# Optimization experiments

Hardware: AMD Instinct MI355X
Metric: run time of the kernel (lower is better)

Reference implementation:

```python
import jax, jax.numpy as jnp
import numpy as np

H, W = 512, 1024            # panorama resolution
GRID = 512                  # occupancy histogram resolution (height=width=512)
ABS_SCALE = 20000.0         # mm, ground-plane extent
UNIT_SCALE = 1000.0         # m -> mm
COUNT_TH = 100.0            # histogram count clamp


def _xyz_sphere(ref_plan):
    # Vectorized version of the original double loop.
    i = np.arange(H, dtype=np.float32)
    j = np.arange(W, dtype=np.float32)
    theta = -np.pi * (i / (H - 1) - 0.5)          # [H]
    phi = np.pi * (2.0 * j / (W - 1) - 1.0)       # [W]
    ct, st = np.cos(theta)[:, None], np.sin(theta)[:, None]   # [H,1]
    cp, sp = np.cos(phi)[None, :], np.sin(phi)[None, :]       # [1,W]
    if ref_plan == 'horizontal':
        P = np.stack([cp * ct, sp * ct, np.broadcast_to(st, (H, W))], 0)
    elif ref_plan == 'vertical':
        P = np.stack([cp * ct, np.broadcast_to(-st, (H, W)), sp * ct], 0)
    else:  # lateral
        P = np.stack([sp * ct, np.broadcast_to(-st, (H, W)), cp * ct], 0)
    return jnp.asarray(P.astype(np.float32))      # [3,H,W]

_SPHERES = [_xyz_sphere(p) for p in ('horizontal', 'vertical', 'lateral')]


def _density_one(depth_hw, sph):
    # depth_hw: [H,W]; sph: [3,H,W]
    ps = depth_hw[None] * sph                               # [3,H,W] 3D points
    xy = ps[:2].reshape(2, -1) * UNIT_SCALE                 # [2,N] mm, (x,y)
    coords = (xy + ABS_SCALE / 2.0) / ABS_SCALE * GRID      # [2,N] in grid units
    coords = jnp.clip(jnp.round(coords), 0.0, GRID - 1).astype(jnp.int32)
    flat = coords[1] * GRID + coords[0]                     # density[y, x]
    hist = jnp.zeros(GRID * GRID, jnp.float32).at[flat].add(1.0)
    hist = jnp.minimum(hist, COUNT_TH)
    hist = hist / jnp.max(hist)
    return hist.reshape(GRID, GRID)


def _density(depth, sph):
    # depth: [B,1,H,W] -> [B,GRID,GRID], batched scatter histogram
    return jax.vmap(_density_one, in_axes=(0, None))(depth[:, 0], sph)


def _inverse_huber(pred, gt):
    # berHu loss: L1 below c = 0.2*max|d|, scaled L2 above.
    diff = jnp.abs(pred - gt)
    c = 0.2 * jnp.max(diff)
    loss = jnp.where(diff <= c, diff, (diff * diff + c * c) / (2.0 * c))
    return jnp.mean(loss)


def setup_inputs() -> dict:
    key = jax.random.key(0)
    k1, k2 = jax.random.split(key)
    # indoor depths in [0, 10) meters so histogram bins are populated
    pred = jax.random.uniform(k1, (16, 1, H, W), jnp.float32) * 10.0
    gt = jax.random.uniform(k2, (16, 1, H, W), jnp.float32) * 10.0
    return {"pred_depth": pred, "gt_depth": gt}


def reference(pred_depth, gt_depth):
    total = jnp.float32(0.0)
    for sph in _SPHERES:  # fixed 3 projection planes
        pred_om = _density(pred_depth, sph)
        gt_om = _density(gt_depth, sph)
        total = total + _inverse_huber(pred_om, gt_om)
    return total
```

## Files before the change

kernel.cpp:

```cpp
#include <hip/hip_runtime.h>

#define PI_F 3.14159265358979323846f

#define MAXZ_OFF_B   24576
#define HIST_OFF_B   32768
#define BINS_OFF_B   25198592

__device__ inline float div20000(float a) {
    const float r = 1.0f / 20000.0f;
    float q0 = a * r;
    float e = fmaf(-20000.0f, q0, a);
    return fmaf(e, r, q0);
}

__device__ inline int bin1(float v) {
    float f = rintf(div20000(v + 10000.0f) * 512.0f);
    return (int)fminf(fmaxf(f, 0.0f), 511.0f);
}

__global__ __launch_bounds__(256) void bin_kernel(
    const float* __restrict__ pred, const float* __restrict__ gt,
    unsigned* __restrict__ bins, unsigned* __restrict__ maxz,
    float* __restrict__ out) {
    __shared__ float sct[4], sst[4];
    const int tid = threadIdx.x, wg = blockIdx.x;
    const int xcd = wg & 7, i4 = (wg >> 3) & 127, hh = wg >> 10;
    const int h = (hh << 3) | xcd;
    if (wg == 0) {
        if (tid < 128) maxz[tid] = 0u;
        if (tid == 128) out[0] = 0.0f;
    }
    if (tid < 4) {
        float fi = (float)(i4 * 4 + tid);
        float theta = -PI_F * (fi / 511.0f - 0.5f);
        sct[tid] = cosf(theta);
        sst[tid] = sinf(theta);
    }
    float cp[4], sp[4];
    #pragma unroll
    for (int k = 0; k < 4; ++k) {
        float fj = (float)(tid * 4 + k);
        float phi = PI_F * ((2.0f * fj) / 1023.0f - 1.0f);
        cp[k] = cosf(phi);
        sp[k] = sinf(phi);
    }
    __syncthreads();
    const float* img = ((h >> 4) ? gt : pred) + ((h & 15) << 19);
    #pragma unroll
    for (int r = 0; r < 4; ++r) {
        const int i = i4 * 4 + r;
        const float4 d4 = *(const float4*)(img + (i << 10) + (tid << 2));
        const float ct = sct[r], st = sst[r];
        uint4 o;
        #pragma unroll
        for (int k = 0; k < 4; ++k) {
            float d = (&d4.x)[k];
            float aA = cp[k] * ct;
            float aB = sp[k] * ct;
            float A = (d * aA) * 1000.0f;
            float B = (d * aB) * 1000.0f;
            float C = (d * (-st)) * 1000.0f;
            int iA = bin1(A), iB = bin1(B), iC = bin1(C);
            (&o.x)[k] = ((unsigned)iC << 18) | ((unsigned)iB << 9) | (unsigned)iA;
        }
        *(uint4*)(bins + ((unsigned)h << 19) + (i << 10) + (tid << 2)) = o;
    }
}

__global__ __launch_bounds__(1024, 8) void scan_kernel(
    const unsigned* __restrict__ bins, unsigned* __restrict__ hp,
    unsigned* __restrict__ maxraw) {
    __shared__ unsigned lh[16384];
    __shared__ unsigned s4[16];
    const int tid = threadIdx.x, wg = blockIdx.x;
    const int xcd = wg & 7, hhi = (wg >> 3) & 3;
    const int X = wg >> 5;
    const int pair = X / 6, idx6 = X % 6;
    const int plane = idx6 >> 1;
    const int band = (idx6 & 1) ? (4 + pair) : (3 - pair);
    const int h = (hhi << 3) | xcd;

    #pragma unroll
    for (int k = 0; k < 4; ++k)
        *(uint4*)&lh[(k << 12) + (tid << 2)] = make_uint4(0, 0, 0, 0);
    __syncthreads();

    int rlo, rhi;
    if (plane == 0) {
        float g = fmaxf(193.0f - 64.0f * band, 64.0f * band - 256.0f);
        float cmin = (g - 4.0f) * (1.0f / 256.0f);
        if (cmin <= 0.0f) { rlo = 0; rhi = 512; }
        else {
            float L = 511.0f * acosf(fminf(cmin, 1.0f)) / PI_F;
            rlo = max(0, (int)floorf(255.5f - L) - 3);
            rhi = min(512, (int)ceilf(255.5f + L) + 4);
        }
    } else if (band == 3) { rlo = 0; rhi = 260; }
    else if (band == 4) { rlo = 0; rhi = 512; }
    else if (band < 3) {
        float smin = (189.0f - 64.0f * band) * (1.0f / 256.0f);
        rlo = 0;
        rhi = min(512, (int)ceilf(511.0f * (0.5f - asinf(smin) / PI_F)) + 4);
    } else {
        float smin = (64.0f * band - 260.0f) * (1.0f / 256.0f);
        rhi = 512;
        rlo = max(0, (int)floorf(511.0f * (0.5f + asinf(smin) / PI_F)) - 4);
    }

    int s1, m1, m2, bsh;
    if (plane == 0)      { s1 = 0; m1 = 0x7FFF; m2 = 0;   bsh = 15; }
    else if (plane == 1) { s1 = 9; m1 = 0x7E00; m2 = 511; bsh = 24; }
    else                 { s1 = 9; m1 = 0x7FFF; m2 = 0;   bsh = 24; }
    const unsigned bandu = (unsigned)band;
    const unsigned* src = bins + ((unsigned)h << 19);

    auto process = [&](uint4 v) {
        #pragma unroll
        for (int k = 0; k < 4; ++k) {
            unsigned b = (&v.x)[k];
            if (((b >> bsh) & 7u) == bandu) {
                unsigned id = ((b >> s1) & m1) | (b & m2);
                atomicAdd(&lh[id >> 1], 1u << ((id & 1u) << 4));
            }
        }
    };

    const int t4 = (tid & 255) << 2;
    const int rof = tid >> 8;
    int r = rlo + rof;
    uint4 cur = make_uint4(0u, 0u, 0u, 0u);
    if (r < rhi) cur = *(const uint4*)&src[(r << 10) + t4];
    for (int rbase = rlo; rbase < rhi; rbase += 4) {
        int rn = rbase + 4 + rof;
        uint4 nxt = make_uint4(0u, 0u, 0u, 0u);
        if (rn < rhi) nxt = *(const uint4*)&src[(rn << 10) + t4];
        if (rbase + rof < rhi) process(cur);
        cur = nxt;
    }
    __syncthreads();

    unsigned m = 0;
    unsigned* gout = hp + ((plane * 32 + h) << 16) + (band << 13);
    #pragma unroll
    for (int k = 0; k < 8; ++k) {
        int w = (k << 10) + tid;
        unsigned v0 = lh[2 * w], v1 = lh[2 * w + 1];
        unsigned c0 = v0 & 65535u, c1 = v0 >> 16;
        unsigned c2 = v1 & 65535u, c3 = v1 >> 16;
        m = max(max(m, max(c0, c1)), max(c2, c3));
        gout[w] = min(c0, 255u) | (min(c1, 255u) << 8) |
                  (min(c2, 255u) << 16) | (min(c3, 255u) << 24);
    }
    #pragma unroll
    for (int o = 32; o; o >>= 1) m = max(m, (unsigned)__shfl_down((int)m, o));
    if ((tid & 63) == 0) s4[tid >> 6] = m;
    __syncthreads();
    if (tid == 0) {
        #pragma unroll
        for (int k = 1; k < 16; ++k) m = max(m, s4[k]);
        atomicMax(&maxraw[plane * 32 + h], m);
    }
}

__device__ inline float blockMaxF(float v) {
    #pragma unroll
    for (int o = 32; o; o >>= 1) v = fmaxf(v, __shfl_down(v, o));
    __shared__ float s[4];
    if ((threadIdx.x & 63) == 0) s[threadIdx.x >> 6] = v;
    __syncthreads();
    if (threadIdx.x == 0) v = fmaxf(fmaxf(s[0], s[1]), fmaxf(s[2], s[3]));
    return v;
}

__device__ inline float blockSumF(float v) {
    #pragma unroll
    for (int o = 32; o; o >>= 1) v += __shfl_down(v, o);
    __shared__ float s[4];
    if ((threadIdx.x & 63) == 0) s[threadIdx.x >> 6] = v;
    __syncthreads();
    if (threadIdx.x == 0) v = (s[0] + s[1]) + (s[2] + s[3]);
    return v;
}

__global__ void maxdiff_kernel(const unsigned* __restrict__ hp,
                               const unsigned* __restrict__ maxraw,
                               unsigned* __restrict__ maxdiff) {
    int blk = blockIdx.x;
    int b = blk & 15, chunk = (blk >> 4) & 15, plane = blk >> 8;
    const unsigned* P = hp + ((plane * 32 + b) << 16) + (chunk << 12);
    const unsigned* G = P + (16 << 16);
    float nP = fminf((float)maxraw[plane * 32 + b], 100.0f);
    float nG = fminf((float)maxraw[plane * 32 + 16 + b], 100.0f);
    float m = 0.0f;
    #pragma unroll
    for (int k = 0; k < 4; ++k) {
        uint4 wp = *(const uint4*)&P[(k << 10) + (threadIdx.x << 2)];
        uint4 wg = *(const uint4*)&G[(k << 10) + (threadIdx.x << 2)];
        #pragma unroll
        for (int w = 0; w < 4; ++w) {
            unsigned up = (&wp.x)[w], ug = (&wg.x)[w];
            #pragma unroll
            for (int s = 0; s < 32; s += 8) {
                float pn = fminf((float)((up >> s) & 255u), 100.0f) / nP;
                float gn = fminf((float)((ug >> s) & 255u), 100.0f) / nG;
                m = fmaxf(m, fabsf(pn - gn));
            }
        }
    }
    m = blockMaxF(m);
    if (threadIdx.x == 0) atomicMax(&maxdiff[plane], __float_as_uint(m));
}

__global__ void loss_kernel(const unsigned* __restrict__ hp,
                            const unsigned* __restrict__ maxraw,
                            const unsigned* __restrict__ maxdiff,
                            float* __restrict__ out) {
    int blk = blockIdx.x;
    int b = blk & 15, chunk = (blk >> 4) & 15, plane = blk >> 8;
    const unsigned* P = hp + ((plane * 32 + b) << 16) + (chunk << 12);
    const unsigned* G = P + (16 << 16);
    float c = 0.2f * __uint_as_float(maxdiff[plane]);
    float nP = fminf((float)maxraw[plane * 32 + b], 100.0f);
    float nG = fminf((float)maxraw[plane * 32 + 16 + b], 100.0f);
    float acc = 0.0f;
    #pragma unroll
    for (int k = 0; k < 4; ++k) {
        uint4 wp = *(const uint4*)&P[(k << 10) + (threadIdx.x << 2)];
        uint4 wg = *(const uint4*)&G[(k << 10) + (threadIdx.x << 2)];
        #pragma unroll
        for (int w = 0; w < 4; ++w) {
            unsigned up = (&wp.x)[w], ug = (&wg.x)[w];
            #pragma unroll
            for (int s = 0; s < 32; s += 8) {
                float pn = fminf((float)((up >> s) & 255u), 100.0f) / nP;
                float gn = fminf((float)((ug >> s) & 255u), 100.0f) / nG;
                float d = fabsf(pn - gn);
                acc += (d <= c) ? d : (d * d + c * c) / (2.0f * c);
            }
        }
    }
    acc = blockSumF(acc);
    if (threadIdx.x == 0) atomicAdd(out, acc / 4194304.0f);
}

extern "C" void kernel_launch(void* const* d_in, const int* in_sizes, int n_in,
                              void* d_out, int out_size, void* d_ws, size_t ws_size,
                              hipStream_t stream) {
    const float* pred = (const float*)d_in[0];
    const float* gt   = (const float*)d_in[1];
    float* out        = (float*)d_out;
    char* ws          = (char*)d_ws;

    unsigned* maxz    = (unsigned*)(ws + MAXZ_OFF_B);
    unsigned* maxraw  = maxz;
    unsigned* maxdiff = maxz + 96;
    unsigned* hp      = (unsigned*)(ws + HIST_OFF_B);
    unsigned* bins    = (unsigned*)(ws + BINS_OFF_B);

    bin_kernel<<<4096, 256, 0, stream>>>(pred, gt, bins, maxz, out);
    scan_kernel<<<768, 1024, 0, stream>>>(bins, hp, maxraw);
    maxdiff_kernel<<<768, 256, 0, stream>>>(hp, maxraw, maxdiff);
    loss_kernel<<<768, 256, 0, stream>>>(hp, maxraw, maxdiff, out);
}
```

Before: 219.8 us.

## Bucket binned indices per plane/band in bin kernel instead of packed bins

The bin kernel now counting-sorts each pixel's three plane indices into 24 plane/band buckets per workgroup, using shared-memory atomic counters, and writes compact 16-bit ids into a per-workgroup region with an offset header. The scan kernel then reads only its own bucket's ids from each of 128 regions instead of streaming whole image rows and filtering by band. This removes the redundant full-row reads and the acos/asin-based row-range logic. In exchange it adds shared atomics and a 48-entry register array in the bin kernel, plus scattered 16-bit global writes.

```diff
diff --git a/kernel.cpp b/kernel.cpp
--- a/kernel.cpp
+++ b/kernel.cpp
@@ -4,7 +4,8 @@
 
 #define MAXZ_OFF_B   24576
 #define HIST_OFF_B   32768
-#define BINS_OFF_B   25198592
+#define BUCK_OFF_B   25198592
+#define REGION_U16   12320
 
 __device__ inline float div20000(float a) {
     const float r = 1.0f / 20000.0f;
@@ -20,9 +21,11 @@
 
 __global__ __launch_bounds__(256) void bin_kernel(
     const float* __restrict__ pred, const float* __restrict__ gt,
-    unsigned* __restrict__ bins, unsigned* __restrict__ maxz,
+    unsigned short* __restrict__ buck, unsigned* __restrict__ maxz,
     float* __restrict__ out) {
     __shared__ float sct[4], sst[4];
+    __shared__ unsigned cnt[24];
+    __shared__ unsigned off[25];
     const int tid = threadIdx.x, wg = blockIdx.x;
     const int xcd = wg & 7, i4 = (wg >> 3) & 127, hh = wg >> 10;
     const int h = (hh << 3) | xcd;
@@ -30,6 +33,7 @@
         if (tid < 128) maxz[tid] = 0u;
         if (tid == 128) out[0] = 0.0f;
     }
+    if (tid < 24) cnt[tid] = 0u;
     if (tid < 4) {
         float fi = (float)(i4 * 4 + tid);
         float theta = -PI_F * (fi / 511.0f - 0.5f);
@@ -46,12 +50,12 @@
     }
     __syncthreads();
     const float* img = ((h >> 4) ? gt : pred) + ((h & 15) << 19);
+    unsigned items[48];
     #pragma unroll
     for (int r = 0; r < 4; ++r) {
         const int i = i4 * 4 + r;
         const float4 d4 = *(const float4*)(img + (i << 10) + (tid << 2));
         const float ct = sct[r], st = sst[r];
-        uint4 o;
         #pragma unroll
         for (int k = 0; k < 4; ++k) {
             float d = (&d4.x)[k];
@@ -61,14 +65,42 @@
             float B = (d * aB) * 1000.0f;
             float C = (d * (-st)) * 1000.0f;
             int iA = bin1(A), iB = bin1(B), iC = bin1(C);
-            (&o.x)[k] = ((unsigned)iC << 18) | ((unsigned)iB << 9) | (unsigned)iA;
-        }
-        *(uint4*)(bins + ((unsigned)h << 19) + (i << 10) + (tid << 2)) = o;
+            unsigned b0 = (unsigned)(iB >> 6);
+            unsigned b1 = 8u + (unsigned)(iC >> 6);
+            unsigned b2 = 16u + (unsigned)(iC >> 6);
+            unsigned id0 = ((unsigned)(iB & 63) << 9) | (unsigned)iA;
+            unsigned id1 = ((unsigned)(iC & 63) << 9) | (unsigned)iA;
+            unsigned id2 = ((unsigned)(iC & 63) << 9) | (unsigned)iB;
+            unsigned r0 = atomicAdd(&cnt[b0], 1u);
+            unsigned r1 = atomicAdd(&cnt[b1], 1u);
+            unsigned r2 = atomicAdd(&cnt[b2], 1u);
+            const int base = (r * 4 + k) * 3;
+            items[base + 0] = (b0 << 27) | (r0 << 15) | id0;
+            items[base + 1] = (b1 << 27) | (r1 << 15) | id1;
+            items[base + 2] = (b2 << 27) | (r2 << 15) | id2;
+        }
+    }
+    __syncthreads();
+    if (tid == 0) {
+        unsigned s = 0;
+        #pragma unroll
+        for (int b = 0; b < 24; ++b) { off[b] = s; s += cnt[b]; }
+        off[24] = s;
+    }
+    __syncthreads();
+    unsigned short* reg = buck + (size_t)wg * REGION_U16;
+    if (tid < 25) reg[tid] = (unsigned short)off[tid];
+    unsigned short* data = reg + 32;
+    #pragma unroll
+    for (int t = 0; t < 48; ++t) {
+        const unsigned it = items[t];
+        data[off[it >> 27] + ((it >> 15) & 4095u)] =
+            (unsigned short)(it & 32767u);
     }
 }
 
 __global__ __launch_bounds__(1024, 8) void scan_kernel(
-    const unsigned* __restrict__ bins, unsigned* __restrict__ hp,
+    const unsigned short* __restrict__ buck, unsigned* __restrict__ hp,
     unsigned* __restrict__ maxraw) {
     __shared__ unsigned lh[16384];
     __shared__ unsigned s4[16];
@@ -79,63 +111,23 @@
     const int plane = idx6 >> 1;
     const int band = (idx6 & 1) ? (4 + pair) : (3 - pair);
     const int h = (hhi << 3) | xcd;
+    const int bucket = plane * 8 + band;
 
     #pragma unroll
     for (int k = 0; k < 4; ++k)
         *(uint4*)&lh[(k << 12) + (tid << 2)] = make_uint4(0, 0, 0, 0);
     __syncthreads();
 
-    int rlo, rhi;
-    if (plane == 0) {
-        float g = fmaxf(193.0f - 64.0f * band, 64.0f * band - 256.0f);
-        float cmin = (g - 4.0f) * (1.0f / 256.0f);
-        if (cmin <= 0.0f) { rlo = 0; rhi = 512; }
-        else {
-            float L = 511.0f * acosf(fminf(cmin, 1.0f)) / PI_F;
-            rlo = max(0, (int)floorf(255.5f - L) - 3);
-            rhi = min(512, (int)ceilf(255.5f + L) + 4);
-        }
-    } else if (band == 3) { rlo = 0; rhi = 260; }
-    else if (band == 4) { rlo = 0; rhi = 512; }
-    else if (band < 3) {
-        float smin = (189.0f - 64.0f * band) * (1.0f / 256.0f);
-        rlo = 0;
-        rhi = min(512, (int)ceilf(511.0f * (0.5f - asinf(smin) / PI_F)) + 4);
-    } else {
-        float smin = (64.0f * band - 260.0f) * (1.0f / 256.0f);
-        rhi = 512;
-        rlo = max(0, (int)floorf(511.0f * (0.5f + asinf(smin) / PI_F)) - 4);
-    }
-
-    int s1, m1, m2, bsh;
-    if (plane == 0)      { s1 = 0; m1 = 0x7FFF; m2 = 0;   bsh = 15; }
-    else if (plane == 1) { s1 = 9; m1 = 0x7E00; m2 = 511; bsh = 24; }
-    else                 { s1 = 9; m1 = 0x7FFF; m2 = 0;   bsh = 24; }
-    const unsigned bandu = (unsigned)band;
-    const unsigned* src = bins + ((unsigned)h << 19);
-
-    auto process = [&](uint4 v) {
-        #pragma unroll
-        for (int k = 0; k < 4; ++k) {
-            unsigned b = (&v.x)[k];
-            if (((b >> bsh) & 7u) == bandu) {
-                unsigned id = ((b >> s1) & m1) | (b & m2);
-                atomicAdd(&lh[id >> 1], 1u << ((id & 1u) << 4));
-            }
-        }
-    };
-
-    const int t4 = (tid & 255) << 2;
-    const int rof = tid >> 8;
-    int r = rlo + rof;
-    uint4 cur = make_uint4(0u, 0u, 0u, 0u);
-    if (r < rhi) cur = *(const uint4*)&src[(r << 10) + t4];
-    for (int rbase = rlo; rbase < rhi; rbase += 4) {
-        int rn = rbase + 4 + rof;
-        uint4 nxt = make_uint4(0u, 0u, 0u, 0u);
-        if (rn < rhi) nxt = *(const uint4*)&src[(rn << 10) + t4];
-        if (rbase + rof < rhi) process(cur);
-        cur = nxt;
+    const int wid = tid >> 6, lane = tid & 63;
+    for (int i4 = wid; i4 < 128; i4 += 16) {
+        const unsigned short* reg =
+            buck + (size_t)(xcd | (i4 << 3) | (hhi << 10)) * REGION_U16;
+        const int lo = reg[bucket], hi = reg[bucket + 1];
+        const unsigned short* data = reg + 32 + lo;
+        for (int j = lane; j < hi - lo; j += 64) {
+            const unsigned id = data[j];
+            atomicAdd(&lh[id >> 1], 1u << ((id & 1u) << 4));
+        }
     }
     __syncthreads();
 
@@ -255,10 +247,10 @@
     unsigned* maxraw  = maxz;
     unsigned* maxdiff = maxz + 96;
     unsigned* hp      = (unsigned*)(ws + HIST_OFF_B);
-    unsigned* bins    = (unsigned*)(ws + BINS_OFF_B);
-
-    bin_kernel<<<4096, 256, 0, stream>>>(pred, gt, bins, maxz, out);
-    scan_kernel<<<768, 1024, 0, stream>>>(bins, hp, maxraw);
+    unsigned short* buck = (unsigned short*)(ws + BUCK_OFF_B);
+
+    bin_kernel<<<4096, 256, 0, stream>>>(pred, gt, buck, maxz, out);
+    scan_kernel<<<768, 1024, 0, stream>>>(buck, hp, maxraw);
     maxdiff_kernel<<<768, 256, 0, stream>>>(hp, maxraw, maxdiff);
     loss_kernel<<<768, 256, 0, stream>>>(hp, maxraw, maxdiff, out);
 }
```

Measured after the change: 294.0 us. 33.8% more time.
